# Kernel optimization log

Measured on AMD Instinct MI355X. Metric: run time of the kernel, lower is better.

Reference implementation:

```python
import jax, jax.numpy as jnp
import numpy as np

B, H, W, C_IN, C_OUT, KH, KW = 32, 56, 56, 128, 256, 3, 3


def setup_inputs() -> dict:
    key = jax.random.key(0)
    k1, k2, k3 = jax.random.split(key, 3)
    x = jax.random.normal(k1, (B, H, W, C_IN), dtype=jnp.float32)
    w = jax.random.normal(k2, (KH, KW, C_IN, C_OUT), dtype=jnp.float32) * 0.05
    b = jax.random.normal(k3, (C_OUT,), dtype=jnp.float32) * 0.05
    return {"x": x, "w": w, "b": b}


def reference(x, w, b):
    # SAME-padded, stride-1 2D conv (math identical to the im2col loop in the
    # original, collapsed into a single conv/GEMM) plus bias.
    out = jax.lax.conv_general_dilated(
        x, w,
        window_strides=(1, 1),
        padding="SAME",
        dimension_numbers=("NHWC", "HWIO", "NHWC"),
    )
    return out + b
```

## Files before the change

kernel.cpp:

```cpp
#include <hip/hip_runtime.h>

#define B_ 32
#define CI 128
#define CO 256
#define K_DIM 1152
#define M_DIM 100352
#define BM 128
#define BN 256
#define BK 32
#define KTILES 36
#define NBUF 3
#define HPAD 58
#define XB_OFF 589824
#define WTBLK 72
#define XPBLK 6728

typedef float          floatx4  __attribute__((ext_vector_type(4)));
typedef unsigned short ushortx8 __attribute__((ext_vector_type(8)));
typedef __bf16         bf16x8   __attribute__((ext_vector_type(8)));

typedef __attribute__((address_space(1))) void gas_void;
typedef __attribute__((address_space(3))) void las_void;
#define GLD16(g, l) __builtin_amdgcn_global_load_lds( \
    (gas_void*)(uintptr_t)(g), (las_void*)(l), 16, 0, 0)

__device__ __forceinline__ unsigned short bf16_rne(float f) {
    unsigned u = __builtin_bit_cast(unsigned, f);
    u += 0x7FFFu + ((u >> 16) & 1u);
    return (unsigned short)(u >> 16);
}

__global__ void prepass_kernel(const float* __restrict__ x,
                               const float* __restrict__ w,
                               unsigned short* __restrict__ xb,
                               unsigned short* __restrict__ wt) {
    __shared__ unsigned short tile[64][65];
    if (blockIdx.x < WTBLK) {
        const int kt = (blockIdx.x % 18) * 64, nt = (blockIdx.x / 18) * 64;
        #pragma unroll
        for (int i = 0; i < 16; ++i) {
            int idx = i * 256 + threadIdx.x;
            int kl = idx >> 6, nl = idx & 63;
            tile[kl][nl] = bf16_rne(w[(size_t)(kt + kl) * CO + nt + nl]);
        }
        __syncthreads();
        #pragma unroll
        for (int i = 0; i < 16; ++i) {
            int idx = i * 256 + threadIdx.x;
            int nl = idx >> 6, kl = idx & 63;
            wt[(size_t)(nt + nl) * K_DIM + kt + kl] = tile[kl][nl];
        }
    } else {
        const int t   = (blockIdx.x - WTBLK) * 256 + threadIdx.x;
        const int pix = t >> 4;
        const int cc  = (t & 15) << 3;
        const int b   = pix / (HPAD * HPAD);
        const int rem = pix % (HPAD * HPAD);
        const int hp  = rem / HPAD, wp = rem % HPAD;
        ushortx8 g = {0, 0, 0, 0, 0, 0, 0, 0};
        if (hp >= 1 && hp <= 56 && wp >= 1 && wp <= 56) {
            const float* s = x + ((size_t)((b * 56 + hp - 1) * 56 + (wp - 1))) * CI + cc;
            floatx4 f0 = ((const floatx4*)s)[0];
            floatx4 f1 = ((const floatx4*)s)[1];
            #pragma unroll
            for (int e = 0; e < 4; ++e) { g[e] = bf16_rne(f0[e]); g[e + 4] = bf16_rne(f1[e]); }
        }
        *(ushortx8*)(xb + (size_t)pix * CI + cc) = g;
    }
}

__global__ __launch_bounds__(512, 4)
void conv_gemm_kernel(const unsigned short* __restrict__ xb,
                      const unsigned short* __restrict__ wt,
                      const float* __restrict__ bias,
                      float* __restrict__ out) {
    __shared__ unsigned short As[NBUF][BM * BK];
    __shared__ unsigned short Bs[NBUF][BN * BK];

    const int tid  = threadIdx.x;
    const int by   = blockIdx.x;
    const int wid  = tid >> 6;
    const int lane = tid & 63;
    const int lrow = lane & 15;
    const int quad = lane >> 4;
    const int wm   = (wid & 1) * 64;
    const int wn   = (wid >> 1) * 64;

    const int rseg = lane >> 2;
    const int cglb = ((lane & 3) - (rseg >> 1)) & 3;

    const int ar = wid * 16 + rseg;
    const int m0 = by * BM + ar;
    const int b0 = m0 / 3136, r0 = m0 % 3136;
    const unsigned short* ag0 = xb + ((size_t)((b0 * HPAD + r0 / 56) * HPAD + r0 % 56)) * CI + cglb * 8;

    const int nr0 = wid * 32 + rseg;
    const unsigned short* bg0 = wt + (size_t)nr0 * K_DIM + cglb * 8;
    const unsigned short* bg1 = bg0 + (size_t)16 * K_DIM;

    const int ldsA  = (wid * 16) * BK;
    const int ldsB0 = (wid * 32) * BK;
    const int ldsB1 = ldsB0 + 16 * BK;

    const int swz = ((quad + (lrow >> 1)) & 3) * 8;
    int a_idx[4], b_idx[4];
    #pragma unroll
    for (int i = 0; i < 4; ++i) {
        a_idx[i] = (wm + i * 16 + lrow) * BK + swz;
        b_idx[i] = (wn + i * 16 + lrow) * BK + swz;
    }

    floatx4 acc[4][4] = {};

    auto stage = [&](int kb, int buf) {
        const int p    = kb >> 2;
        const int c0   = (kb & 3) << 5;
        const int aoff = (p / 3 * HPAD + p % 3) * CI + c0;
        const int boff = kb * BK;
        GLD16(ag0 + aoff, &As[buf][ldsA]);
        GLD16(bg0 + boff, &Bs[buf][ldsB0]);
        GLD16(bg1 + boff, &Bs[buf][ldsB1]);
    };

    auto compute = [&](int buf) {
        ushortx8 arv[4], brv[4];
        #pragma unroll
        for (int mi = 0; mi < 4; ++mi) arv[mi] = *(const ushortx8*)&As[buf][a_idx[mi]];
        #pragma unroll
        for (int ni = 0; ni < 4; ++ni) brv[ni] = *(const ushortx8*)&Bs[buf][b_idx[ni]];
        __builtin_amdgcn_s_setprio(1);
        #pragma unroll
        for (int mi = 0; mi < 4; ++mi)
            #pragma unroll
            for (int ni = 0; ni < 4; ++ni)
                acc[mi][ni] = __builtin_amdgcn_mfma_f32_16x16x32_bf16(
                    __builtin_bit_cast(bf16x8, arv[mi]),
                    __builtin_bit_cast(bf16x8, brv[ni]),
                    acc[mi][ni], 0, 0, 0);
        __builtin_amdgcn_s_setprio(0);
    };

    stage(0, 0);
    stage(1, 1);

#define ITER(T, BC, BS)                                                  \
    do {                                                                 \
        if ((T) < KTILES - 1) asm volatile("s_waitcnt vmcnt(3)" ::: "memory"); \
        else                  asm volatile("s_waitcnt vmcnt(0)" ::: "memory"); \
        __builtin_amdgcn_s_barrier();                                    \
        asm volatile("" ::: "memory");                                   \
        if ((T) + 2 < KTILES) stage((T) + 2, (BS));                      \
        compute((BC));                                                   \
    } while (0)

    #pragma unroll 1
    for (int tt = 0; tt < KTILES; tt += 3) {
        ITER(tt + 0, 0, 2);
        ITER(tt + 1, 1, 0);
        ITER(tt + 2, 2, 1);
    }
#undef ITER

    float bv[4];
    #pragma unroll
    for (int ni = 0; ni < 4; ++ni)
        bv[ni] = bias[wn + ni * 16 + lrow];

    #pragma unroll
    for (int mi = 0; mi < 4; ++mi) {
        #pragma unroll
        for (int r = 0; r < 4; ++r) {
            const int row = by * BM + wm + mi * 16 + quad * 4 + r;
            float* o = out + (size_t)row * CO + wn + lrow;
            #pragma unroll
            for (int ni = 0; ni < 4; ++ni)
                o[ni * 16] = acc[mi][ni][r] + bv[ni];
        }
    }
}

extern "C" void kernel_launch(void* const* d_in, const int* in_sizes, int n_in,
                              void* d_out, int out_size, void* d_ws, size_t ws_size,
                              hipStream_t stream) {
    (void)in_sizes; (void)n_in; (void)out_size; (void)ws_size;
    const float* x    = (const float*)d_in[0];
    const float* w    = (const float*)d_in[1];
    const float* bias = (const float*)d_in[2];
    float* out = (float*)d_out;

    unsigned short* wt = (unsigned short*)d_ws;
    unsigned short* xb = (unsigned short*)((char*)d_ws + XB_OFF);

    prepass_kernel<<<dim3(WTBLK + XPBLK), dim3(256), 0, stream>>>(x, w, xb, wt);
    conv_gemm_kernel<<<dim3(M_DIM / BM), dim3(512), 0, stream>>>(xb, wt, bias, out);
}
```

Baseline: 212.0 us.

## Double M tile to 256 with BK64 double-buffered split-phase pipeline

Doubles the GEMM block tile to 256x256 with BK=64, so each wave holds an 8x4 MFMA accumulator grid. The K loop is restructured into a two-buffer scheme with half-tile phases that interleave LDS reads, async global-to-LDS staging and MFMA bursts. Block IDs are remapped so that the eight XCDs each take contiguous M ranges. The larger tile raises reuse of the weight operand and halves the block count, at the cost of more registers and LDS, occupancy lowered to 2 blocks per CU, and 392 blocks that may leave CUs idle in the tail.

After: 204.7 us. -3.4%, faster.

```diff
diff --git a/kernel.cpp b/kernel.cpp
--- a/kernel.cpp
+++ b/kernel.cpp
@@ -5,15 +5,15 @@
 #define CO 256
 #define K_DIM 1152
 #define M_DIM 100352
-#define BM 128
+#define BM 256
 #define BN 256
-#define BK 32
-#define KTILES 36
-#define NBUF 3
+#define BK 64
+#define KT 18
 #define HPAD 58
 #define XB_OFF 589824
 #define WTBLK 72
 #define XPBLK 6728
+#define GRID_M 392
 
 typedef float          floatx4  __attribute__((ext_vector_type(4)));
 typedef unsigned short ushortx8 __attribute__((ext_vector_type(8)));
@@ -69,97 +69,107 @@
     }
 }
 
-__global__ __launch_bounds__(512, 4)
+__global__ __launch_bounds__(512, 2)
 void conv_gemm_kernel(const unsigned short* __restrict__ xb,
                       const unsigned short* __restrict__ wt,
                       const float* __restrict__ bias,
                       float* __restrict__ out) {
-    __shared__ unsigned short As[NBUF][BM * BK];
-    __shared__ unsigned short Bs[NBUF][BN * BK];
+    __shared__ unsigned short As[2][2][BM * 32];
+    __shared__ unsigned short Bs[2][2][BN * 32];
 
     const int tid  = threadIdx.x;
-    const int by   = blockIdx.x;
+    const int bid  = blockIdx.x;
+    const int by   = (bid & 7) * (GRID_M / 8) + (bid >> 3);
     const int wid  = tid >> 6;
     const int lane = tid & 63;
     const int lrow = lane & 15;
     const int quad = lane >> 4;
-    const int wm   = (wid & 1) * 64;
+    const int wm   = (wid & 1) * 128;
     const int wn   = (wid >> 1) * 64;
 
     const int rseg = lane >> 2;
     const int cglb = ((lane & 3) - (rseg >> 1)) & 3;
 
-    const int ar = wid * 16 + rseg;
-    const int m0 = by * BM + ar;
-    const int b0 = m0 / 3136, r0 = m0 % 3136;
-    const unsigned short* ag0 = xb + ((size_t)((b0 * HPAD + r0 / 56) * HPAD + r0 % 56)) * CI + cglb * 8;
-
-    const int nr0 = wid * 32 + rseg;
-    const unsigned short* bg0 = wt + (size_t)nr0 * K_DIM + cglb * 8;
-    const unsigned short* bg1 = bg0 + (size_t)16 * K_DIM;
-
-    const int ldsA  = (wid * 16) * BK;
-    const int ldsB0 = (wid * 32) * BK;
-    const int ldsB1 = ldsB0 + 16 * BK;
+    const unsigned short* aga[2];
+    const unsigned short* bga[2];
+    #pragma unroll
+    for (int g = 0; g < 2; ++g) {
+        const int m0 = by * BM + g * 128 + wid * 16 + rseg;
+        const int b0 = m0 / 3136, r0 = m0 % 3136;
+        aga[g] = xb + ((size_t)((b0 * HPAD + r0 / 56) * HPAD + r0 % 56)) * CI + cglb * 8;
+        const int n0 = g * 128 + wid * 16 + rseg;
+        bga[g] = wt + (size_t)n0 * K_DIM + cglb * 8;
+    }
+    const int wbase = wid * 512;
 
     const int swz = ((quad + (lrow >> 1)) & 3) * 8;
-    int a_idx[4], b_idx[4];
-    #pragma unroll
-    for (int i = 0; i < 4; ++i) {
-        a_idx[i] = (wm + i * 16 + lrow) * BK + swz;
-        b_idx[i] = (wn + i * 16 + lrow) * BK + swz;
-    }
-
-    floatx4 acc[4][4] = {};
-
-    auto stage = [&](int kb, int buf) {
-        const int p    = kb >> 2;
-        const int c0   = (kb & 3) << 5;
-        const int aoff = (p / 3 * HPAD + p % 3) * CI + c0;
-        const int boff = kb * BK;
-        GLD16(ag0 + aoff, &As[buf][ldsA]);
-        GLD16(bg0 + boff, &Bs[buf][ldsB0]);
-        GLD16(bg1 + boff, &Bs[buf][ldsB1]);
-    };
-
-    auto compute = [&](int buf) {
-        ushortx8 arv[4], brv[4];
-        #pragma unroll
-        for (int mi = 0; mi < 4; ++mi) arv[mi] = *(const ushortx8*)&As[buf][a_idx[mi]];
-        #pragma unroll
-        for (int ni = 0; ni < 4; ++ni) brv[ni] = *(const ushortx8*)&Bs[buf][b_idx[ni]];
+    int arow[8], brow[4];
+    #pragma unroll
+    for (int i = 0; i < 8; ++i) arow[i] = (wm + i * 16 + lrow) * 32 + swz;
+    #pragma unroll
+    for (int i = 0; i < 4; ++i) brow[i] = (wn + i * 16 + lrow) * 32 + swz;
+
+    floatx4 acc[8][4] = {};
+
+    auto stageA = [&](int t1, int kk, int sb) {
+        const int p    = t1 >> 1;
+        const int aoff = (p / 3 * HPAD + p % 3) * CI + (t1 & 1) * 64 + kk * 32;
+        GLD16(aga[0] + aoff, &As[sb][kk][wbase]);
+        GLD16(aga[1] + aoff, &As[sb][kk][4096 + wbase]);
+    };
+    auto stageB = [&](int t1, int kk, int sb) {
+        const int boff = t1 * 64 + kk * 32;
+        GLD16(bga[0] + boff, &Bs[sb][kk][wbase]);
+        GLD16(bga[1] + boff, &Bs[sb][kk][4096 + wbase]);
+    };
+
+    ushortx8 bfr[4], afr[4];
+    auto rdB = [&](int buf, int kk) {
+        #pragma unroll
+        for (int ni = 0; ni < 4; ++ni) bfr[ni] = *(const ushortx8*)&Bs[buf][kk][brow[ni]];
+    };
+    auto rdA = [&](int buf, int kk, int h) {
+        #pragma unroll
+        for (int i = 0; i < 4; ++i) afr[i] = *(const ushortx8*)&As[buf][kk][arow[h * 4 + i]];
+    };
+    auto mm = [&](int h) {
         __builtin_amdgcn_s_setprio(1);
         #pragma unroll
-        for (int mi = 0; mi < 4; ++mi)
+        for (int i = 0; i < 4; ++i)
             #pragma unroll
             for (int ni = 0; ni < 4; ++ni)
-                acc[mi][ni] = __builtin_amdgcn_mfma_f32_16x16x32_bf16(
-                    __builtin_bit_cast(bf16x8, arv[mi]),
-                    __builtin_bit_cast(bf16x8, brv[ni]),
-                    acc[mi][ni], 0, 0, 0);
+                acc[h * 4 + i][ni] = __builtin_amdgcn_mfma_f32_16x16x32_bf16(
+                    __builtin_bit_cast(bf16x8, afr[i]),
+                    __builtin_bit_cast(bf16x8, bfr[ni]),
+                    acc[h * 4 + i][ni], 0, 0, 0);
         __builtin_amdgcn_s_setprio(0);
     };
 
-    stage(0, 0);
-    stage(1, 1);
-
-#define ITER(T, BC, BS)                                                  \
-    do {                                                                 \
-        if ((T) < KTILES - 1) asm volatile("s_waitcnt vmcnt(3)" ::: "memory"); \
-        else                  asm volatile("s_waitcnt vmcnt(0)" ::: "memory"); \
-        __builtin_amdgcn_s_barrier();                                    \
-        asm volatile("" ::: "memory");                                   \
-        if ((T) + 2 < KTILES) stage((T) + 2, (BS));                      \
-        compute((BC));                                                   \
-    } while (0)
+    stageA(0, 0, 0); stageB(0, 0, 0); stageA(0, 1, 0); stageB(0, 1, 0);
 
     #pragma unroll 1
-    for (int tt = 0; tt < KTILES; tt += 3) {
-        ITER(tt + 0, 0, 2);
-        ITER(tt + 1, 1, 0);
-        ITER(tt + 2, 2, 1);
-    }
-#undef ITER
+    for (int t = 0; t < KT; ++t) {
+        const int buf  = t & 1, sb = buf ^ 1;
+        const int t1   = t + 1;
+        const bool more = t1 < KT;
+        asm volatile("s_waitcnt vmcnt(4)\n\ts_barrier" ::: "memory");
+        rdB(buf, 0); rdA(buf, 0, 0);
+        if (more) stageA(t1, 0, sb);
+        mm(0);
+        asm volatile("s_barrier" ::: "memory");
+        rdA(buf, 0, 1);
+        if (more) stageB(t1, 0, sb);
+        mm(1);
+        if (more) asm volatile("s_waitcnt vmcnt(4)\n\ts_barrier" ::: "memory");
+        else      asm volatile("s_waitcnt vmcnt(0)\n\ts_barrier" ::: "memory");
+        rdB(buf, 1); rdA(buf, 1, 0);
+        if (more) stageA(t1, 1, sb);
+        mm(0);
+        asm volatile("s_barrier" ::: "memory");
+        rdA(buf, 1, 1);
+        if (more) stageB(t1, 1, sb);
+        mm(1);
+    }
 
     float bv[4];
     #pragma unroll
@@ -167,7 +177,7 @@
         bv[ni] = bias[wn + ni * 16 + lrow];
 
     #pragma unroll
-    for (int mi = 0; mi < 4; ++mi) {
+    for (int mi = 0; mi < 8; ++mi) {
         #pragma unroll
         for (int r = 0; r < 4; ++r) {
             const int row = by * BM + wm + mi * 16 + quad * 4 + r;
@@ -192,5 +202,5 @@
     unsigned short* xb = (unsigned short*)((char*)d_ws + XB_OFF);
 
     prepass_kernel<<<dim3(WTBLK + XPBLK), dim3(256), 0, stream>>>(x, w, xb, wt);
-    conv_gemm_kernel<<<dim3(M_DIM / BM), dim3(512), 0, stream>>>(xb, wt, bias, out);
-}
+    conv_gemm_kernel<<<dim3(GRID_M), dim3(512), 0, stream>>>(xb, wt, bias, out);
+}
```
